# Optimization experiments

Hardware: AMD Instinct MI355X
Metric: run time of the kernel (lower is better)

## Reference

```python
import jax, jax.numpy as jnp
import numpy as np

NUM_HEADS = 8


def setup_inputs() -> dict:
    key = jax.random.key(0)
    ks = jax.random.split(key, 7)
    B, D, N = 16, 512, 2048
    sc = 1.0 / np.sqrt(D)
    return {
        "X_Query": jax.random.normal(ks[0], (B, D, N), jnp.float32),
        "X_Key": jax.random.normal(ks[1], (B, D, N), jnp.float32),
        "X_Value": jax.random.normal(ks[2], (B, D, N), jnp.float32),
        "W_q": jax.random.normal(ks[3], (D, D), jnp.float32) * sc,
        "W_k": jax.random.normal(ks[4], (D, D), jnp.float32) * sc,
        "W_v": jax.random.normal(ks[5], (D, D), jnp.float32) * sc,
        "W_o": jax.random.normal(ks[6], (D, D), jnp.float32) * sc,
    }


def _proj(W, x):
    # Conv1d(D, D, kernel_size=1, bias=False) == channel matmul
    return jnp.einsum('oi,bin->bon', W, x)


def _split_heads(x, h):
    # torch: cat(x.chunk(h, dim=-1), dim=0) -> (h, B, D, N/h) stacked layout
    B, D, N = x.shape
    return x.reshape(B, D, h, N // h).transpose(2, 0, 1, 3)


def _mha(XQ, XK, XV, Wq, Wk, Wv, Wo):
    B, D, N = XQ.shape
    h = NUM_HEADS
    Nh = N // h
    q = _split_heads(_proj(Wq, XQ), h)  # (h, B, D, Nh)
    k = _split_heads(_proj(Wk, XK), h)
    v = _split_heads(_proj(Wv, XV), h)
    # scores over the CHANNEL axis: (h, B, D, D), scaled by sqrt(d_k)=sqrt(Nh)
    scores = jnp.einsum('hbdn,hben->hbde', q, k) / jnp.sqrt(jnp.asarray(Nh, q.dtype))
    p = jax.nn.softmax(scores, axis=-1)
    out = jnp.einsum('hbde,hben->hbdn', p, v)  # (h, B, D, Nh)
    # torch: cat(chunks, dim=0) inverse -> cat along dim=-1
    attn_heads = out.transpose(1, 2, 0, 3).reshape(B, D, N)
    return _proj(Wo, XQ - attn_heads)


def reference(X_Query, X_Key, X_Value, W_q, W_k, W_v, W_o):
    return _mha(X_Query, X_Key, X_Value, W_q, W_k, W_v, W_o)
```

## Files before the change

kernel.cpp:

```cpp
#include <hip/hip_runtime.h>
#include <hip/hip_bf16.h>

#define DD  512
#define NN  2048
#define BB  16
#define NHD 256

typedef unsigned short u16;
typedef __attribute__((ext_vector_type(4))) float f32x4;
typedef __attribute__((ext_vector_type(8))) short s16x8;
typedef __attribute__((ext_vector_type(4))) short s16x4;
typedef __attribute__((ext_vector_type(4))) u16   u16x4;

static __device__ __forceinline__ u16 f2bf(float f) {
  __hip_bfloat16 h = __float2bfloat16(f);
  return *reinterpret_cast<u16*>(&h);
}
static __device__ __forceinline__ float bf2f(u16 u) {
  union { unsigned int i; float f; } v; v.i = ((unsigned int)u) << 16; return v.f;
}
static __device__ __forceinline__ f32x4 mfma_bf16(s16x8 a, s16x8 b, f32x4 c) {
  return __builtin_amdgcn_mfma_f32_16x16x32_bf16(a, b, c, 0, 0, 0);
}
static __device__ __forceinline__ void gload_lds16(const u16* g, u16* l) {
  __builtin_amdgcn_global_load_lds(
      (const __attribute__((address_space(1))) unsigned int*)g,
      (__attribute__((address_space(3))) unsigned int*)l, 16, 0, 0);
}
static __device__ __forceinline__ void barrier_raw() {
  __builtin_amdgcn_sched_barrier(0);
  __builtin_amdgcn_s_barrier();
  __builtin_amdgcn_sched_barrier(0);
}
#define WAITCNT(s) do { asm volatile("s_waitcnt " s ::: "memory"); \
                        __builtin_amdgcn_sched_barrier(0); } while (0)

__global__ __launch_bounds__(256) void k_cvt_w(const float* __restrict__ w0,
                                               const float* __restrict__ w1,
                                               const float* __restrict__ w2,
                                               const float* __restrict__ w3,
                                               u16* __restrict__ out) {
  const float* srcs[4] = {w0, w1, w2, w3};
  const float* s = srcs[blockIdx.y];
  u16* o = out + (size_t)blockIdx.y * (DD * DD);
  int idx = blockIdx.x * 256 + threadIdx.x;
  float4 v = *(const float4*)(s + (size_t)idx * 4);
  u16x4 u = {f2bf(v.x), f2bf(v.y), f2bf(v.z), f2bf(v.w)};
  *(u16x4*)(o + (size_t)idx * 4) = u;
}

__global__ __launch_bounds__(256) void k_transpose3(const float* __restrict__ x0,
                                                    const float* __restrict__ x1,
                                                    const float* __restrict__ x2,
                                                    u16* __restrict__ o0,
                                                    u16* __restrict__ o1,
                                                    u16* __restrict__ o2) {
  __shared__ float t[64][65];
  const int tid = threadIdx.x;
  const int z = blockIdx.z, which = z >> 4, b = z & 15;
  const float* X = which == 0 ? x0 : (which == 1 ? x1 : x2);
  u16*       XT = which == 0 ? o0 : (which == 1 ? o1 : o2);
  const int n0 = blockIdx.x * 64, d0 = blockIdx.y * 64;
  const float* Xb = X + ((size_t)b * DD + d0) * NN + n0;
#pragma unroll
  for (int i = 0; i < 4; ++i) {
    int r = (tid >> 4) + i * 16;
    int c = (tid & 15) * 4;
    float4 v = *(const float4*)(Xb + (size_t)r * NN + c);
    t[r][c] = v.x; t[r][c + 1] = v.y; t[r][c + 2] = v.z; t[r][c + 3] = v.w;
  }
  __syncthreads();
  u16* Ob = XT + ((size_t)b * NN + n0) * DD + d0;
#pragma unroll
  for (int i = 0; i < 4; ++i) {
    int n = (tid >> 4) + i * 16;
    int d = (tid & 15) * 4;
    u16x4 u = {f2bf(t[d][n]), f2bf(t[d + 1][n]), f2bf(t[d + 2][n]), f2bf(t[d + 3][n])};
    *(u16x4*)(Ob + (size_t)n * DD + d) = u;
  }
}

#define GEMM_STAGE(Ag, lda, Bg, ldb, buf, kt)                                   \
  {                                                                             \
    _Pragma("unroll")                                                           \
    for (int j = 0; j < 4; ++j) {                                               \
      int s = j * 256 + w * 64 + lane;                                          \
      int row = s >> 3, u = s & 7;                                              \
      int col = ((u ^ (row & 7)) * 8);                                          \
      gload_lds16(Ag + (size_t)row * lda + (kt) * 64 + col, &Ab[buf][s * 8]);   \
      gload_lds16(Bg + (size_t)row * ldb + (kt) * 64 + col, &Bb[buf][s * 8]);   \
    }                                                                           \
  }

#define GEMM_COMPUTE(buf)                                                       \
  {                                                                             \
    _Pragma("unroll")                                                           \
    for (int ks = 0; ks < 2; ++ks) {                                            \
      s16x8 av[4], bv[4];                                                       \
      _Pragma("unroll")                                                         \
      for (int m = 0; m < 4; ++m) {                                             \
        int row = wm + m * 16 + r;                                              \
        av[m] = *(const s16x8*)&Ab[buf][row * 64 + (((ks * 4 + g) ^ (row & 7)) * 8)]; \
      }                                                                         \
      _Pragma("unroll")                                                         \
      for (int nf = 0; nf < 4; ++nf) {                                          \
        int row = wn + nf * 16 + r;                                             \
        bv[nf] = *(const s16x8*)&Bb[buf][row * 64 + (((ks * 4 + g) ^ (row & 7)) * 8)]; \
      }                                                                         \
      _Pragma("unroll")                                                         \
      for (int m = 0; m < 4; ++m)                                               \
        _Pragma("unroll")                                                       \
        for (int nf = 0; nf < 4; ++nf)                                          \
          acc[m][nf] = mfma_bf16(av[m], bv[nf], acc[m][nf]);                    \
    }                                                                           \
  }

#define GEMM_PREAMBLE                                                           \
  __shared__ __align__(16) u16 Ab[2][128 * 64];                                 \
  __shared__ __align__(16) u16 Bb[2][128 * 64];                                 \
  const int tid = threadIdx.x;                                                  \
  const int lane = tid & 63, w = tid >> 6;                                      \
  const int wm = (w >> 1) * 64, wn = (w & 1) * 64;                              \
  const int r = lane & 15, g = lane >> 4;                                       \
  f32x4 acc[4][4] = {};

#define GEMM_MAINLOOP(Ag, lda, Bg, ldb, nkt)                                    \
  GEMM_STAGE(Ag, lda, Bg, ldb, 0, 0);                                           \
  __syncthreads();                                                              \
  for (int kt = 0; kt < (nkt) - 1; ++kt) {                                      \
    GEMM_STAGE(Ag, lda, Bg, ldb, (kt & 1) ^ 1, kt + 1);                         \
    GEMM_COMPUTE(kt & 1);                                                       \
    __syncthreads();                                                            \
  }                                                                             \
  GEMM_COMPUTE(((nkt) - 1) & 1);

template <typename OUT_T>
__global__ __launch_bounds__(256) void k_gemm_nt(
    const u16* __restrict__ A, long long a_bs, int lda,
    const u16* __restrict__ B, long long b_bs, int ldb,
    OUT_T* __restrict__ C, long long c_bs, int ldc, int K) {
  GEMM_PREAMBLE
  const int m0 = blockIdx.x * 128, n0 = blockIdx.y * 128;
  const u16* Ag = A + (size_t)blockIdx.z * a_bs + (size_t)m0 * lda;
  const u16* Bg = B + (size_t)blockIdx.z * b_bs + (size_t)n0 * ldb;
  const int nkt = K >> 6;
  GEMM_MAINLOOP(Ag, lda, Bg, ldb, nkt);

  OUT_T* Cg = C + (size_t)blockIdx.z * c_bs;
#pragma unroll
  for (int m = 0; m < 4; ++m)
#pragma unroll
    for (int nf = 0; nf < 4; ++nf)
#pragma unroll
      for (int j = 0; j < 4; ++j) {
        int row = m0 + wm + m * 16 + g * 4 + j;
        int col = n0 + wn + nf * 16 + r;
        float v = acc[m][nf][j];
        if constexpr (sizeof(OUT_T) == 2) Cg[(size_t)row * ldc + col] = f2bf(v);
        else                              Cg[(size_t)row * ldc + col] = v;
      }
}

__global__ __launch_bounds__(512, 4) void k_attn_fused(
    const u16* __restrict__ Qdn, const u16* __restrict__ Kdn,
    const u16* __restrict__ VT,  const u16* __restrict__ XqT,
    u16* __restrict__ And) {
  __shared__ __align__(16) u16 L[26880];
  u16* Kr = L;
  u16* Vr = L + 12288;
  u16* Ps = L + 24576;

  const int tid = threadIdx.x;
  const int lane = tid & 63, w = tid >> 6;
  const int r = lane & 15, g = lane >> 4;
  const int dq = w >> 1, eh = w & 1;
  const int nq = w >> 1, dh = w & 1;
  const int bid = blockIdx.x;
  const int dt = bid >> 7, hb = bid & 127;
  const int h = hb & 7, b = hb >> 3;
  const int d0 = dt * 64, hn0 = h * NHD;

  const u16* Qg = Qdn + ((size_t)b * DD + d0) * NN + hn0;
  const u16* Kg = Kdn + ((size_t)b * DD) * NN + hn0;
  const u16* Vg = VT + ((size_t)b * NN + hn0) * DD;

  auto stage_k = [&](int s) {
    const int e0 = (s >> 1) * 32, n0 = (s & 1) * 128;
    u16* dst = Kr + (s % 3) * 4096;
    int row = tid >> 4, u = tid & 15;
    gload_lds16(Kg + (size_t)(e0 + row) * NN + n0 + ((u ^ (row & 7)) * 8), dst + tid * 8);
  };
  auto stage_v = [&](int t) {
    const int e0 = (t >> 1) * 32, j = t & 1;
    u16* dst = Vr + (t % 3) * 4096;
    int rl = tid >> 2, u = tid & 3;
    int gn = (rl >> 5) * 64 + j * 32 + (rl & 31);
    gload_lds16(Vg + (size_t)gn * DD + e0 + ((u ^ (rl & 3)) * 8), dst + tid * 8);
  };

#pragma unroll
  for (int jj = 0; jj < 4; ++jj) {
    int s = jj * 512 + tid;
    int row = s >> 5, u = s & 31;
    gload_lds16(Qg + (size_t)row * NN + ((u ^ (row & 7)) * 8), L + s * 8);
  }
  WAITCNT("vmcnt(0)");
  barrier_raw();
  s16x8 qf[8];
  {
    const int qrow = dq * 16 + r;
#pragma unroll
    for (int k2 = 0; k2 < 8; ++k2)
      qf[k2] = *(const s16x8*)&L[qrow * 256 + (((k2 * 4 + g) ^ (qrow & 7)) * 8)];
  }
  WAITCNT("lgkmcnt(0)");
  barrier_raw();
  stage_k(0); stage_v(0); stage_k(1);

  float psum[4] = {};
  f32x4 acc_o[2][2][2] = {};

  for (int et = 0; et < 16; ++et) {
    f32x4 acc_s = {};
#pragma unroll
    for (int cn = 0; cn < 2; ++cn) {
      const int s = et * 2 + cn;
      if (cn == 0)      WAITCNT("vmcnt(2)");
      else if (et < 15) WAITCNT("vmcnt(2)");
      else              WAITCNT("vmcnt(1)");
      barrier_raw();
      if (s + 1 < 32) stage_v(s + 1);
      if (s + 2 < 32) stage_k(s + 2);
      const u16* kb = Kr + (s % 3) * 4096;
      const int rowe = eh * 16 + r;
      __builtin_amdgcn_s_setprio(1);
#pragma unroll
      for (int kq = 0; kq < 4; ++kq) {
        s16x8 bv = *(const s16x8*)&kb[rowe * 128 + (((kq * 4 + g) ^ (rowe & 7)) * 8)];
        acc_s = mfma_bf16(qf[cn * 4 + kq], bv, acc_s);
      }
      __builtin_amdgcn_s_setprio(0);
      WAITCNT("lgkmcnt(0)");
    }
#pragma unroll
    for (int j = 0; j < 4; ++j) {
      int rowd = dq * 16 + g * 4 + j;
      int cole = eh * 16 + r;
      float p = __expf(acc_s[j] * 0.0625f);
      psum[j] += p;
      Ps[rowd * 36 + cole] = f2bf(p);
    }
    WAITCNT("lgkmcnt(0)");
    if (et < 15) WAITCNT("vmcnt(3)");
    else         WAITCNT("vmcnt(0)");
    barrier_raw();
#pragma unroll
    for (int j = 0; j < 2; ++j) {
      const u16* vb = Vr + ((et * 2 + j) % 3) * 4096;
      s16x8 pb[2];
#pragma unroll
      for (int nf = 0; nf < 2; ++nf) {
        int rowd = dh * 32 + nf * 16 + r;
        s16x4 plo = *(const s16x4*)&Ps[rowd * 36 + g * 8];
        s16x4 phi = *(const s16x4*)&Ps[rowd * 36 + g * 8 + 4];
        pb[nf] = __builtin_shufflevector(plo, phi, 0, 1, 2, 3, 4, 5, 6, 7);
      }
      __builtin_amdgcn_s_setprio(1);
#pragma unroll
      for (int ms = 0; ms < 2; ++ms) {
        int rl = nq * 32 + ms * 16 + r;
        s16x8 av = *(const s16x8*)((const char*)vb + rl * 64 + ((g * 16) ^ ((rl & 3) << 4)));
        acc_o[j][ms][0] = mfma_bf16(av, pb[0], acc_o[j][ms][0]);
        acc_o[j][ms][1] = mfma_bf16(av, pb[1], acc_o[j][ms][1]);
      }
      __builtin_amdgcn_s_setprio(0);
    }
    WAITCNT("lgkmcnt(0)");
    barrier_raw();
  }

  float* rs = (float*)L;
#pragma unroll
  for (int j = 0; j < 4; ++j) {
    float v = psum[j];
    v += __shfl_xor(v, 1);
    v += __shfl_xor(v, 2);
    v += __shfl_xor(v, 4);
    v += __shfl_xor(v, 8);
    if (r == 0) rs[w * 16 + g * 4 + j] = v;
  }
  __syncthreads();
  if (tid < 64) {
    int dqi = tid >> 4, i = tid & 15;
    rs[128 + tid] = 1.0f / (rs[(dqi * 2) * 16 + i] + rs[(dqi * 2 + 1) * 16 + i]);
  }
  __syncthreads();

  const u16* Xg = XqT + ((size_t)b * NN + hn0) * DD + d0;
  u16* Ag = And + ((size_t)b * NN + hn0) * DD + d0;
#pragma unroll
  for (int j = 0; j < 2; ++j)
#pragma unroll
    for (int ms = 0; ms < 2; ++ms)
#pragma unroll
      for (int nf = 0; nf < 2; ++nf) {
        const int dc = dh * 32 + nf * 16 + r;
        const float inv = rs[128 + dc];
#pragma unroll
        for (int jj = 0; jj < 4; ++jj) {
          const int npos = nq * 64 + j * 32 + ms * 16 + g * 4 + jj;
          float o = acc_o[j][ms][nf][jj] * inv;
          float xq = bf2f(Xg[(size_t)npos * DD + dc]);
          Ag[(size_t)npos * DD + dc] = f2bf(xq - o);
        }
      }
}

extern "C" void kernel_launch(void* const* d_in, const int* in_sizes, int n_in,
                              void* d_out, int out_size, void* d_ws, size_t ws_size,
                              hipStream_t stream) {
  const float* Xq = (const float*)d_in[0];
  const float* Xk = (const float*)d_in[1];
  const float* Xv = (const float*)d_in[2];
  const float* Wq = (const float*)d_in[3];
  const float* Wk = (const float*)d_in[4];
  const float* Wv = (const float*)d_in[5];
  const float* Wo = (const float*)d_in[6];
  float* out = (float*)d_out;

  char* ws = (char*)d_ws;
  const size_t MB = 1024 * 1024;
  u16* Wb  = (u16*)ws;
  u16* XqT = (u16*)(ws + 2 * MB);
  u16* XvT = (u16*)(ws + 34 * MB);
  u16* And = XvT;
  u16* Qdn = (u16*)(ws + 66 * MB);
  u16* XkT = (u16*)(ws + 98 * MB);
  u16* VTb = (u16*)d_out;
  u16* Kdn = (u16*)d_out + (size_t)BB * NN * DD;

  k_cvt_w<<<dim3(256, 4), 256, 0, stream>>>(Wq, Wk, Wv, Wo, Wb);

  k_transpose3<<<dim3(NN / 64, DD / 64, BB * 3), 256, 0, stream>>>(
      Xq, Xk, Xv, XqT, XkT, XvT);

  k_gemm_nt<u16><<<dim3(NN / 128, DD / 128, BB), 256, 0, stream>>>(
      XvT, (long long)NN * DD, DD,
      Wb + 2 * DD * DD, 0, DD,
      VTb, (long long)NN * DD, DD, DD);
  k_gemm_nt<u16><<<dim3(DD / 128, NN / 128, BB), 256, 0, stream>>>(
      Wb, 0, DD,
      XqT, (long long)NN * DD, DD,
      Qdn, (long long)DD * NN, NN, DD);
  k_gemm_nt<u16><<<dim3(DD / 128, NN / 128, BB), 256, 0, stream>>>(
      Wb + 1 * DD * DD, 0, DD,
      XkT, (long long)NN * DD, DD,
      Kdn, (long long)DD * NN, NN, DD);

  k_attn_fused<<<dim3(1024), 512, 0, stream>>>(Qdn, Kdn, VTb, XqT, And);

  k_gemm_nt<float><<<dim3(DD / 128, NN / 128, BB), 256, 0, stream>>>(
      Wb + 3 * DD * DD, 0, DD,
      And, (long long)NN * DD, DD,
      out, (long long)DD * NN, NN, DD);
}
```

Before: 249.0 us.

## Restructure attention K/V staging into double-buffered per-tile loads with fewer barriers

Changes the fused attention kernel from a triple-buffered pipeline over half-tiles (K and V staged in 32-channel x 128-column pieces) to a double-buffered pipeline that stages a full 32-row K tile and the matching V tile once per iteration. This removes one barrier and one wait pair per iteration and lets the score MFMAs run over all 8 k-steps back to back. The P fragment loads are hoisted out of the V loop, and the et loop is fully unrolled. LDS use rises from about 53 KB to about 70 KB per block, which may lower occupancy, and the prefetch for the next tile now starts later, after the score computation.

```diff
diff --git a/kernel.cpp b/kernel.cpp
--- a/kernel.cpp
+++ b/kernel.cpp
@@ -165,10 +165,10 @@
     const u16* __restrict__ Qdn, const u16* __restrict__ Kdn,
     const u16* __restrict__ VT,  const u16* __restrict__ XqT,
     u16* __restrict__ And) {
-  __shared__ __align__(16) u16 L[26880];
+  __shared__ __align__(16) u16 L[35072];
   u16* Kr = L;
-  u16* Vr = L + 12288;
-  u16* Ps = L + 24576;
+  u16* Vr = L + 16384;
+  u16* Ps = L + 32768;
 
   const int tid = threadIdx.x;
   const int lane = tid & 63, w = tid >> 6;
@@ -184,18 +184,25 @@
   const u16* Kg = Kdn + ((size_t)b * DD) * NN + hn0;
   const u16* Vg = VT + ((size_t)b * NN + hn0) * DD;
 
-  auto stage_k = [&](int s) {
-    const int e0 = (s >> 1) * 32, n0 = (s & 1) * 128;
-    u16* dst = Kr + (s % 3) * 4096;
-    int row = tid >> 4, u = tid & 15;
-    gload_lds16(Kg + (size_t)(e0 + row) * NN + n0 + ((u ^ (row & 7)) * 8), dst + tid * 8);
+  auto stage_ket = [&](int et) {
+    u16* dst = Kr + (et & 1) * 8192;
+    const u16* src = Kg + (size_t)(et * 32) * NN;
+#pragma unroll
+    for (int j = 0; j < 2; ++j) {
+      int s = j * 512 + tid;
+      int row = s >> 5, u = s & 31;
+      gload_lds16(src + (size_t)row * NN + ((u ^ (row & 7)) * 8), dst + s * 8);
+    }
   };
-  auto stage_v = [&](int t) {
-    const int e0 = (t >> 1) * 32, j = t & 1;
-    u16* dst = Vr + (t % 3) * 4096;
+  auto stage_vet = [&](int et) {
+    u16* dst = Vr + (et & 1) * 8192;
     int rl = tid >> 2, u = tid & 3;
-    int gn = (rl >> 5) * 64 + j * 32 + (rl & 31);
-    gload_lds16(Vg + (size_t)gn * DD + e0 + ((u ^ (rl & 3)) * 8), dst + tid * 8);
+#pragma unroll
+    for (int j = 0; j < 2; ++j) {
+      int gn = (rl >> 5) * 64 + j * 32 + (rl & 31);
+      gload_lds16(Vg + (size_t)gn * DD + et * 32 + ((u ^ (rl & 3)) * 8),
+                  dst + j * 4096 + tid * 8);
+    }
   };
 
 #pragma unroll
@@ -215,33 +222,28 @@
   }
   WAITCNT("lgkmcnt(0)");
   barrier_raw();
-  stage_k(0); stage_v(0); stage_k(1);
+  stage_ket(0); stage_vet(0);
 
   float psum[4] = {};
   f32x4 acc_o[2][2][2] = {};
 
+#pragma unroll
   for (int et = 0; et < 16; ++et) {
+    WAITCNT("vmcnt(2)");
+    barrier_raw();
     f32x4 acc_s = {};
-#pragma unroll
-    for (int cn = 0; cn < 2; ++cn) {
-      const int s = et * 2 + cn;
-      if (cn == 0)      WAITCNT("vmcnt(2)");
-      else if (et < 15) WAITCNT("vmcnt(2)");
-      else              WAITCNT("vmcnt(1)");
-      barrier_raw();
-      if (s + 1 < 32) stage_v(s + 1);
-      if (s + 2 < 32) stage_k(s + 2);
-      const u16* kb = Kr + (s % 3) * 4096;
-      const int rowe = eh * 16 + r;
-      __builtin_amdgcn_s_setprio(1);
-#pragma unroll
-      for (int kq = 0; kq < 4; ++kq) {
-        s16x8 bv = *(const s16x8*)&kb[rowe * 128 + (((kq * 4 + g) ^ (rowe & 7)) * 8)];
-        acc_s = mfma_bf16(qf[cn * 4 + kq], bv, acc_s);
-      }
-      __builtin_amdgcn_s_setprio(0);
-      WAITCNT("lgkmcnt(0)");
-    }
+    const u16* kb = Kr + (et & 1) * 8192;
+    const int rowe = eh * 16 + r;
+    __builtin_amdgcn_s_setprio(1);
+#pragma unroll
+    for (int kq = 0; kq < 8; ++kq) {
+      s16x8 bv = *(const s16x8*)&kb[rowe * 256 + (((kq * 4 + g) ^ (rowe & 7)) * 8)];
+      acc_s = mfma_bf16(qf[kq], bv, acc_s);
+    }
+    __builtin_amdgcn_s_setprio(0);
+    WAITCNT("lgkmcnt(0)");
+    barrier_raw();
+    if (et + 1 < 16) { stage_ket(et + 1); stage_vet(et + 1); }
 #pragma unroll
     for (int j = 0; j < 4; ++j) {
       int rowd = dq * 16 + g * 4 + j;
@@ -251,21 +253,21 @@
       Ps[rowd * 36 + cole] = f2bf(p);
     }
     WAITCNT("lgkmcnt(0)");
-    if (et < 15) WAITCNT("vmcnt(3)");
+    if (et < 15) WAITCNT("vmcnt(4)");
     else         WAITCNT("vmcnt(0)");
     barrier_raw();
+    s16x8 pb[2];
+#pragma unroll
+    for (int nf = 0; nf < 2; ++nf) {
+      int rowd = dh * 32 + nf * 16 + r;
+      s16x4 plo = *(const s16x4*)&Ps[rowd * 36 + g * 8];
+      s16x4 phi = *(const s16x4*)&Ps[rowd * 36 + g * 8 + 4];
+      pb[nf] = __builtin_shufflevector(plo, phi, 0, 1, 2, 3, 4, 5, 6, 7);
+    }
+    __builtin_amdgcn_s_setprio(1);
 #pragma unroll
     for (int j = 0; j < 2; ++j) {
-      const u16* vb = Vr + ((et * 2 + j) % 3) * 4096;
-      s16x8 pb[2];
-#pragma unroll
-      for (int nf = 0; nf < 2; ++nf) {
-        int rowd = dh * 32 + nf * 16 + r;
-        s16x4 plo = *(const s16x4*)&Ps[rowd * 36 + g * 8];
-        s16x4 phi = *(const s16x4*)&Ps[rowd * 36 + g * 8 + 4];
-        pb[nf] = __builtin_shufflevector(plo, phi, 0, 1, 2, 3, 4, 5, 6, 7);
-      }
-      __builtin_amdgcn_s_setprio(1);
+      const u16* vb = Vr + (et & 1) * 8192 + j * 4096;
 #pragma unroll
       for (int ms = 0; ms < 2; ++ms) {
         int rl = nq * 32 + ms * 16 + r;
@@ -273,12 +275,12 @@
         acc_o[j][ms][0] = mfma_bf16(av, pb[0], acc_o[j][ms][0]);
         acc_o[j][ms][1] = mfma_bf16(av, pb[1], acc_o[j][ms][1]);
       }
-      __builtin_amdgcn_s_setprio(0);
-    }
+    }
+    __builtin_amdgcn_s_setprio(0);
     WAITCNT("lgkmcnt(0)");
-    barrier_raw();
-  }
-
+  }
+
+  barrier_raw();
   float* rs = (float*)L;
 #pragma unroll
   for (int j = 0; j < 4; ++j) {
```

New measurement: 267.1 us. 7.3% more time.
